# Optimization experiments

Measured on AMD Instinct MI355X. Metric: run time of the kernel, lower is better.

## Reference

```python
import jax, jax.numpy as jnp
import numpy as np

IMG_SIZE = 224
ALPHA = 100.0  # hardcoded softmax temperature in knnsearch_t_grad


def _sqdist(a, b):
    # (B,N,C),(B,M,C) -> (B,N,M) squared euclidean distances
    return (jnp.sum(a * a, -1)[:, :, None]
            - 2.0 * jnp.einsum('bnc,bmc->bnm', a, b)
            + jnp.sum(b * b, -1)[:, None, :])


def _cdist(a, b):
    return jnp.sqrt(jnp.maximum(_sqdist(a, b), 1e-12))


def proj2img(pc, img_offset):
    # faithful jax port of GraphDeformLoss_Neural_Partial.proj2img
    B, N, _ = pc.shape
    pc_max = pc.max(axis=1)              # (B,3)
    pc_min_full = pc.min(axis=1)         # (B,3)
    pc_range = pc_max - pc_min_full
    grid_size = pc_range[:, :2].max(axis=-1) / (IMG_SIZE - 3)   # (B,)
    pc_min = pc_min_full[:, None, :2]                            # (B,1,2)
    gs = grid_size[:, None, None]
    idx_xy = jnp.floor((pc[:, :, :2] - pc_min) / gs)             # (B,N,2)
    # densify each point into a 5x5 neighborhood of pixels
    idx_dense = (idx_xy[:, :, None, :] + img_offset[None, None]).reshape(B, N * 25, 2) + 1.0
    center = jnp.floor((idx_dense.max(axis=1) + idx_dense.min(axis=1)) / 2.0)  # (B,2)
    offset = IMG_SIZE / 2.0 - center - 1.0                       # (B,2) = (offset_x, offset_y)
    idx_off = idx_dense + offset[:, None, :]
    # boundary correction as in the torch code, plus clip for safety
    idx_off = idx_off + (idx_off < 0).astype(jnp.float32) - (idx_off > IMG_SIZE - 1).astype(jnp.float32)
    idx_off = jnp.clip(idx_off, 0, IMG_SIZE - 1)
    f_dense = jnp.repeat(jnp.repeat(pc[:, :, None, 2:3], 25, axis=2).reshape(B, N * 25, 1), 3, axis=-1)
    flat = (idx_off[..., 0] * IMG_SIZE + idx_off[..., 1]).astype(jnp.int32)   # (B,N*25)
    out = jax.vmap(lambda f, i: jax.ops.segment_sum(f, i, num_segments=IMG_SIZE * IMG_SIZE))(f_dense, flat)
    img = out.reshape(B, IMG_SIZE, IMG_SIZE, 3).transpose(0, 3, 1, 2)  # (B,3,H,W)
    return jax.nn.sigmoid(img)


def setup_inputs() -> dict:
    key = jax.random.key(0)
    k1, k2, k3, k4 = jax.random.split(key, 4)
    B, N, M, C = 4, 4995, 4995, 128
    off = jnp.array([[i, j] for i in range(-2, 3) for j in range(-2, 3)], dtype=jnp.float32)
    return {
        'verts1': jax.random.normal(k1, (B, N, 3), jnp.float32),
        'verts2': jax.random.normal(k2, (B, M, 3), jnp.float32),
        'feat1': jax.random.normal(k3, (B, N, C), jnp.float32),
        'feat2': jax.random.normal(k4, (B, M, C), jnp.float32),
        'img_offset': off,
        'k': 10,
    }


def reference(verts1, verts2, feat1, feat2, img_offset, k):
    # knnsearch_t_grad: soft correspondence from feature-space cdist + softmax
    d_feat = _cdist(feat1, feat2)                               # (B,N,M)
    Pi_12 = jax.nn.softmax(-ALPHA * d_feat, axis=-1)
    verts12 = jnp.einsum('bnm,bmc->bnc', Pi_12, verts2)         # pulled-back points (B,N,3)
    # chamfer (squared distances, as chamfer_3DDist); partial: take dist1 branch (N<=M)
    d2 = _sqdist(verts12, verts2)
    self_rec_loss = jnp.mean(jnp.min(d2, axis=-1))
    # knn_grad + index_points: gather k-NN features on source cloud
    d2_11 = _sqdist(verts1, verts1)
    _, idx11 = jax.lax.top_k(-d2_11, k)                         # (B,N,k) nearest
    feat1_conv = jax.vmap(lambda p, i: p[i])(feat1, idx11)      # (B,N,k,C)
    deform_feat_loss = jnp.mean((feat1_conv - feat1[:, :, None, :]) ** 2)
    # point-to-image projection loss
    img1 = proj2img(verts12, img_offset)
    img2 = proj2img(verts2, img_offset)
    img_loss = jnp.mean((img1 - img2) ** 2)
    return self_rec_loss + img_loss + deform_feat_loss
```

## Files before the change

kernel.cpp:

```cpp
#include <hip/hip_runtime.h>
#include <math.h>

#define BB 4
#define NN 4995
#define CC 128
#define IMG 224
#define IMGP (IMG*IMG)
#define ALPHA_F 100.0f
#define SPLITS 8
#define COLS_PER_SPLIT 640
#define RBLK 40
#define NG 158
#define NTAP (2*BB*NN*25)
#define NREP 4
#define TKCAP 256

#define SM_SCALE 20813.6898f
#define NEG2S   -41627.3796f
#define EPS_S    2.08136898e-8f

#define OFF_V12    0
#define OFF_FN1    60000
#define OFF_V1Q    81000
#define OFF_V2Q    161000
#define OFF_C2Q    241000
#define OFF_PART   321000
#define OFF_IMG1   1121000
#define OFF_IMG2   1321704
#define OFF_ACC    1522408
#define OFF_STATS  1522792
#define OFF_PADQ   1522920
#define OFF_F2H    1523000
#define OFF_F2L    2818000
#define OFF_IMGR   4113000
#define WS_NEED_REP ((size_t)5719000*sizeof(float))
#define ZERO_START OFF_IMG1
#define ZERO_FLOATS (1522920 - OFF_IMG1)

typedef short v8s  __attribute__((ext_vector_type(8)));
typedef float v16f __attribute__((ext_vector_type(16)));

#if __has_builtin(__builtin_amdgcn_exp2f)
__device__ __forceinline__ float fast_exp2(float x){ return __builtin_amdgcn_exp2f(x); }
#else
__device__ __forceinline__ float fast_exp2(float x){ float r; asm("v_exp_f32 %0, %1" : "=v"(r) : "v"(x)); return r; }
#endif
#if __has_builtin(__builtin_amdgcn_sqrtf)
__device__ __forceinline__ float fast_sqrt(float x){ return __builtin_amdgcn_sqrtf(x); }
#else
__device__ __forceinline__ float fast_sqrt(float x){ float r; asm("v_sqrt_f32 %0, %1" : "=v"(r) : "v"(x)); return r; }
#endif

__device__ __forceinline__ float wave_min(float v){
#pragma unroll
  for (int off=32; off; off>>=1) v = fminf(v, __shfl_xor(v, off));
  return v;
}
__device__ __forceinline__ float wave_sum(float v){
#pragma unroll
  for (int off=32; off; off>>=1) v += __shfl_xor(v, off);
  return v;
}

__device__ __forceinline__ int pack_bf_hi(float a, float b){
  return (int)__builtin_amdgcn_perm(__float_as_uint(b), __float_as_uint(a), 0x07060302u);
}

__device__ __forceinline__ void cvt_hilo(float4 a, float4 c, int4& hi, int4& lo){
  float hx=__uint_as_float(__float_as_uint(a.x)&0xffff0000u);
  float hy=__uint_as_float(__float_as_uint(a.y)&0xffff0000u);
  float hz=__uint_as_float(__float_as_uint(a.z)&0xffff0000u);
  float hw=__uint_as_float(__float_as_uint(a.w)&0xffff0000u);
  float gx=__uint_as_float(__float_as_uint(c.x)&0xffff0000u);
  float gy=__uint_as_float(__float_as_uint(c.y)&0xffff0000u);
  float gz=__uint_as_float(__float_as_uint(c.z)&0xffff0000u);
  float gw=__uint_as_float(__float_as_uint(c.w)&0xffff0000u);
  hi = make_int4(pack_bf_hi(a.x,a.y), pack_bf_hi(a.z,a.w),
                 pack_bf_hi(c.x,c.y), pack_bf_hi(c.z,c.w));
  lo = make_int4(pack_bf_hi(a.x-hx,a.y-hy), pack_bf_hi(a.z-hz,a.w-hw),
                 pack_bf_hi(c.x-gx,c.y-gy), pack_bf_hi(c.z-gz,c.w-gw));
}

__device__ __forceinline__ v8s i4_to_s8(int4 v){
  union { int4 i; v8s s; } u; u.i = v; return u.s;
}

__device__ __forceinline__ void gld_lds16(const void* g, void* l){
  __builtin_amdgcn_global_load_lds((const __attribute__((address_space(1))) void*)g,
                                   (__attribute__((address_space(3))) void*)l, 16, 0, 0);
}

__device__ __forceinline__ unsigned int fkey(float f){
  unsigned int u = __float_as_uint(f);
  return ((int)u < 0) ? ~u : (u ^ 0x80000000u);
}

__global__ __launch_bounds__(256) void k_norms(const float* __restrict__ verts1, const float* __restrict__ verts2,
                        const float* __restrict__ feat1, const float* __restrict__ feat2,
                        float* __restrict__ ws) {
  int gt = blockIdx.x*blockDim.x + threadIdx.x;
  int i = gt >> 2, sub = gt & 3;
  if (i >= BB*NN) return;
  const float4* fa = (const float4*)(feat1 + (size_t)i*CC) + sub*8;
  const float4* fb = (const float4*)(feat2 + (size_t)i*CC) + sub*8;
  float s1=0.f, s2=0.f;
#pragma unroll
  for (int k=0;k<8;k++){
    float4 t = fa[k];
    s1 = fmaf(t.x,t.x,s1); s1 = fmaf(t.y,t.y,s1); s1 = fmaf(t.z,t.z,s1); s1 = fmaf(t.w,t.w,s1);
    float4 u = fb[k];
    s2 = fmaf(u.x,u.x,s2); s2 = fmaf(u.y,u.y,s2); s2 = fmaf(u.z,u.z,s2); s2 = fmaf(u.w,u.w,s2);
  }
  s1 += __shfl_xor(s1,1); s1 += __shfl_xor(s1,2);
  s2 += __shfl_xor(s2,1); s2 += __shfl_xor(s2,2);
  if (sub == 0){
    float x=verts1[(size_t)i*3], y=verts1[(size_t)i*3+1], z=verts1[(size_t)i*3+2];
    ((float4*)(ws+OFF_V1Q))[i] = make_float4(x,y,z, x*x+y*y+z*z);
    float x2=verts2[(size_t)i*3], y2=verts2[(size_t)i*3+1], z2=verts2[(size_t)i*3+2];
    ((float4*)(ws+OFF_V2Q))[i] = make_float4(x2,y2,z2, x2*x2+y2*y2+z2*z2);
    ((float4*)(ws+OFF_C2Q))[i] = make_float4(x2,y2,z2, SM_SCALE*s2);
    ws[OFF_FN1+i] = SM_SCALE*s1;
  }
  if (gt == 0)
    *((float4*)(ws+OFF_PADQ)) = make_float4(0.f,0.f,0.f,1e30f);
}

__global__ __launch_bounds__(256) void k_conv(const float* __restrict__ feat2, float* __restrict__ ws) {
  int g = blockIdx.x, b = blockIdx.y;
  int t = threadIdx.x;
  int q = t >> 5, c32 = t & 31;
  int col = g*32 + c32; if (col > NN-1) col = NN-1;
  const float4* src = (const float4*)(feat2 + ((size_t)(b*NN + col))*CC) + q*4;
  float4 v0 = src[0], v1 = src[1], v2 = src[2], v3 = src[3];
  short* f2h = (short*)(ws + OFF_F2H);
  short* f2l = (short*)(ws + OFF_F2L);
  size_t base = ((size_t)(b*NG + g))*4096 + (size_t)q*512 + c32*8;
  int4 hi, lo;
  cvt_hilo(v0, v1, hi, lo);
  *(int4*)&f2h[base] = hi;  *(int4*)&f2l[base] = lo;
  cvt_hilo(v2, v3, hi, lo);
  *(int4*)&f2h[base + 256] = hi;  *(int4*)&f2l[base + 256] = lo;
}

__global__ __launch_bounds__(256) void k_stageA(const float* __restrict__ feat1,
      float* __restrict__ ws) {
  __shared__ __align__(16) short Bbuf[2][4096];
  __shared__ __align__(16) float colq[768*4];

  int rblk  = blockIdx.x;
  int split = blockIdx.y;
  int b     = blockIdx.z;
  int rowBase = rblk*128;
  int colBase = split*COLS_PER_SPLIT;
  int colEnd  = colBase + COLS_PER_SPLIT; if (colEnd > NN) colEnd = NN;
  int nct = (colEnd - colBase + 63) >> 6;
  int nst = nct << 2;

  int t    = threadIdx.x;
  int w    = t >> 6;
  int lane = t & 63;
  int half = lane >> 5;
  int m32  = lane & 31;

  const float* f1b = feat1 + (size_t)b*NN*CC;
  const short* f2h = (const short*)(ws + OFF_F2H);
  const short* f2l = (const short*)(ws + OFF_F2L);
  const float4* c2q = (const float4*)(ws + OFF_C2Q) + (size_t)b*NN;
  const float4* padq = (const float4*)(ws + OFF_PADQ);

#pragma unroll
  for (int r=0; r<3; r++){
    int col = colBase + r*256 + t;
    const float4* src = (col < NN) ? (c2q + col) : padq;
    gld_lds16(src, &colq[(r*256 + w*64)*4]);
  }

  size_t f2base = (((size_t)(b*NG) + (colBase>>5) + (w>>1)) << 12) + (size_t)((t&127)*8);

  {
    short* d = &Bbuf[0][0] + w*512;
    gld_lds16(f2h + f2base, d);
    gld_lds16(f2l + f2base, d + 2048);
  }

  int nrow = rowBase + w*32 + m32;
  int nclamp = nrow > NN-1 ? NN-1 : nrow;
  float sn = ws[OFF_FN1 + (size_t)b*NN + nclamp];
  const float4* ar = (const float4*)(f1b + (size_t)nclamp*CC) + (half<<1);
  v8s Afh[8], Afl[8];
#pragma unroll
  for (int sl=0; sl<8; ++sl){
    float4 v0 = ar[sl*4], v1 = ar[sl*4+1];
    int4 hi, lo;
    cvt_hilo(v0, v1, hi, lo);
    Afh[sl] = i4_to_s8(hi); Afl[sl] = i4_to_s8(lo);
  }

  __syncthreads();

  float mm = INFINITY, S = 0.f, Vx = 0.f, Vy = 0.f, Vz = 0.f;

  for (int ci = 0; ci < nct; ci++){
    v16f acc0, acc1;
#pragma unroll
    for (int i=0;i<16;i++){ acc0[i]=0.f; acc1[i]=0.f; }

#pragma unroll
    for (int kt = 0; kt < 4; kt++){
      int s = (ci<<2) + kt;
      if (s+1 < nst){
        int s1 = s+1;
        size_t so = f2base + ((size_t)(s1>>2)<<13) + ((size_t)(s1&3)<<10);
        short* d = &Bbuf[0][0] + ((s1&1)<<12) + w*512;
        gld_lds16(f2h + so, d);
        gld_lds16(f2l + so, d + 2048);
      }
      const short* Bh = &Bbuf[0][0] + ((s&1)<<12);
      const short* Bl = Bh + 2048;
#pragma unroll
      for (int kh=0; kh<2; kh++){
        int fo = (kh<<9) + (half<<8) + (m32<<3);
        v8s a0h = *(const v8s*)&Bh[fo];
        v8s a0l = *(const v8s*)&Bl[fo];
        v8s a1h = *(const v8s*)&Bh[1024+fo];
        v8s a1l = *(const v8s*)&Bl[1024+fo];
        v8s b1h = Afh[kt*2+kh];
        v8s b1l = Afl[kt*2+kh];
        __builtin_amdgcn_s_setprio(1);
        acc0 = __builtin_amdgcn_mfma_f32_32x32x16_bf16(a0h, b1h, acc0, 0,0,0);
        acc0 = __builtin_amdgcn_mfma_f32_32x32x16_bf16(a0h, b1l, acc0, 0,0,0);
        acc0 = __builtin_amdgcn_mfma_f32_32x32x16_bf16(a0l, b1h, acc0, 0,0,0);
        acc1 = __builtin_amdgcn_mfma_f32_32x32x16_bf16(a1h, b1h, acc1, 0,0,0);
        acc1 = __builtin_amdgcn_mfma_f32_32x32x16_bf16(a1h, b1l, acc1, 0,0,0);
        acc1 = __builtin_amdgcn_mfma_f32_32x32x16_bf16(a1l, b1h, acc1, 0,0,0);
        __builtin_amdgcn_s_setprio(0);
      }
      __syncthreads();
    }

    int cb4 = ci<<8;
    float Mt = INFINITY;
#pragma unroll
    for (int reg=0; reg<16; reg++){
      int cp0 = (reg&3) + 8*(reg>>2) + 4*half;
      float f0 = colq[cb4 + cp0*4 + 3];
      float d0 = fmaf(NEG2S, acc0[reg], sn) + f0;
      float p0 = fast_sqrt(fmaxf(d0, EPS_S));
      acc0[reg] = p0; Mt = fminf(Mt, p0);
      float f1v = colq[cb4 + (cp0+32)*4 + 3];
      float d1 = fmaf(NEG2S, acc1[reg], sn) + f1v;
      float p1 = fast_sqrt(fmaxf(d1, EPS_S));
      acc1[reg] = p1; Mt = fminf(Mt, p1);
    }
    float mn = fminf(mm, Mt);
    float sc = fast_exp2(mn - mm);
    float se=0.f, sx=0.f, sy=0.f, sz=0.f;
#pragma unroll
    for (int reg=0; reg<16; reg++){
      int cp0 = (reg&3) + 8*(reg>>2) + 4*half;
      float4 q0 = *(const float4*)&colq[cb4 + cp0*4];
      float e0 = fast_exp2(mn - acc0[reg]);
      se += e0; sx=fmaf(e0,q0.x,sx); sy=fmaf(e0,q0.y,sy); sz=fmaf(e0,q0.z,sz);
      float4 q1 = *(const float4*)&colq[cb4 + (cp0+32)*4];
      float e1 = fast_exp2(mn - acc1[reg]);
      se += e1; sx=fmaf(e1,q1.x,sx); sy=fmaf(e1,q1.y,sy); sz=fmaf(e1,q1.z,sz);
    }
    S  = fmaf(S,  sc, se);
    Vx = fmaf(Vx, sc, sx);
    Vy = fmaf(Vy, sc, sy);
    Vz = fmaf(Vz, sc, sz);
    mm = mn;
  }

  {
    float m2  = __shfl_xor(mm, 32);
    float S2  = __shfl_xor(S,  32);
    float Vx2 = __shfl_xor(Vx, 32);
    float Vy2 = __shfl_xor(Vy, 32);
    float Vz2 = __shfl_xor(Vz, 32);
    float M = fminf(mm, m2);
    float c1 = fast_exp2(M - mm), c2 = fast_exp2(M - m2);
    float Sf  = S*c1  + S2*c2;
    float Vxf = Vx*c1 + Vx2*c2;
    float Vyf = Vy*c1 + Vy2*c2;
    float Vzf = Vz*c1 + Vz2*c2;
    if (half==0 && nrow < NN){
      float* p = ws + OFF_PART + ((size_t)(b*NN+nrow)*SPLITS + split)*5;
      p[0]=M; p[1]=Sf; p[2]=Vxf; p[3]=Vyf; p[4]=Vzf;
    }
  }
}

__global__ void k_combine(float* __restrict__ ws) {
  int row = blockIdx.x*blockDim.x + threadIdx.x;
  if (row >= BB*NN) return;
  const float* p = ws + OFF_PART + (size_t)row*SPLITS*5;
  float mm = INFINITY;
#pragma unroll
  for (int s=0;s<SPLITS;s++) mm = fminf(mm, p[s*5]);
  float S=0.f,Vx=0.f,Vy=0.f,Vz=0.f;
#pragma unroll
  for (int s=0;s<SPLITS;s++){
    float sc = fast_exp2(mm - p[s*5]);
    S  += p[s*5+1]*sc; Vx += p[s*5+2]*sc; Vy += p[s*5+3]*sc; Vz += p[s*5+4]*sc;
  }
  ws[OFF_V12+(size_t)row*3+0]=Vx/S;
  ws[OFF_V12+(size_t)row*3+1]=Vy/S;
  ws[OFF_V12+(size_t)row*3+2]=Vz/S;
}

__global__ __launch_bounds__(256) void k_selfrec(float* __restrict__ ws) {
  int rblk = blockIdx.x, b = blockIdx.y;
  int lane = threadIdx.x & 63, w = threadIdx.x >> 6;
  int r0 = rblk*16 + w*4;
  const float4* v2q = (const float4*)(ws + OFF_V2Q) + (size_t)b*NN;
  const float* v12 = ws + OFF_V12 + (size_t)b*NN*3;
  float xr[4], yr[4], zr[4], sar[4]; bool val[4];
#pragma unroll
  for (int j=0;j<4;j++){
    int n = r0+j; val[j] = (n < NN); int nc = val[j] ? n : NN-1;
    float x=v12[(size_t)nc*3], y=v12[(size_t)nc*3+1], z=v12[(size_t)nc*3+2];
    sar[j]=x*x+y*y+z*z;
    xr[j]=-2.0f*x; yr[j]=-2.0f*y; zr[j]=-2.0f*z;
  }
  float mn0=INFINITY, mn1=INFINITY, mn2=INFINITY, mn3=INFINITY;
  for (int m=lane; m<NN; m+=64) {
    float4 q = v2q[m];
    mn0 = fminf(mn0, fmaf(xr[0],q.x, fmaf(yr[0],q.y, fmaf(zr[0],q.z, q.w))));
    mn1 = fminf(mn1, fmaf(xr[1],q.x, fmaf(yr[1],q.y, fmaf(zr[1],q.z, q.w))));
    mn2 = fminf(mn2, fmaf(xr[2],q.x, fmaf(yr[2],q.y, fmaf(zr[2],q.z, q.w))));
    mn3 = fminf(mn3, fmaf(xr[3],q.x, fmaf(yr[3],q.y, fmaf(zr[3],q.z, q.w))));
  }
  mn0 = wave_min(mn0); mn1 = wave_min(mn1); mn2 = wave_min(mn2); mn3 = wave_min(mn3);
  float s = (val[0]?(mn0+sar[0]):0.f) + (val[1]?(mn1+sar[1]):0.f)
          + (val[2]?(mn2+sar[2]):0.f) + (val[3]?(mn3+sar[3]):0.f);
  if (lane==0)
    atomicAdd(((double*)(ws+OFF_ACC)) + ((rblk*4 + w) & 63), (double)s);
}

__global__ __launch_bounds__(256, 4) void k_topk(const float* __restrict__ feat1,
        const int* __restrict__ kptr, float* __restrict__ ws) {
  __shared__ unsigned int keybuf[4*256];
  __shared__ unsigned long long cand[4*TKCAP];
  __shared__ int scnt[4];
  __shared__ float tfs[4];
  __shared__ int sel[4][16];
  __shared__ float rs[4];
  int t = threadIdx.x;
  int lane = t & 63, wid = t >> 6;
  int b = blockIdx.y;
  int n0 = blockIdx.x*4;
  int kk = *kptr; if (kk > 16) kk = 16; if (kk < 1) kk = 1;

  const float4* v1q = (const float4*)(ws + OFF_V1Q) + (size_t)b*NN;
  float mx[4], my2[4], mz[4], sa_unused;
  (void)sa_unused;
#pragma unroll
  for (int j=0;j<4;j++){
    int n = n0+j; if (n > NN-1) n = NN-1;
    float4 me = v1q[n];
    mx[j]=-2.0f*me.x; my2[j]=-2.0f*me.y; mz[j]=-2.0f*me.z;
  }
  if (t < 4) scnt[t] = 0;

  float e2[20][4];
  float mn[4] = {INFINITY, INFINITY, INFINITY, INFINITY};
#pragma unroll
  for (int i=0;i<19;i++){
    int m = t + 256*i;
    float4 q = v1q[m];
#pragma unroll
    for (int j=0;j<4;j++){
      float d = fmaf(mx[j], q.x, fmaf(my2[j], q.y, fmaf(mz[j], q.z, q.w)));
      e2[i][j] = d; mn[j] = fminf(mn[j], d);
    }
  }
  {
    int m = t + 256*19;
    bool ok = (m < NN);
    float4 q = v1q[ok ? m : NN-1];
#pragma unroll
    for (int j=0;j<4;j++){
      float d = fmaf(mx[j], q.x, fmaf(my2[j], q.y, fmaf(mz[j], q.z, q.w)));
      d = ok ? d : 1e30f;
      e2[19][j] = d; mn[j] = fminf(mn[j], d);
    }
  }

#pragma unroll
  for (int j=0;j<4;j++)
    keybuf[j*256 + t] = fkey(mn[j]) >> 16;
  __syncthreads();

  {
    unsigned int k0 = keybuf[wid*256 + lane];
    unsigned int k1 = keybuf[wid*256 + 64 + lane];
    unsigned int k2 = keybuf[wid*256 + 128 + lane];
    unsigned int k3 = keybuf[wid*256 + 192 + lane];
    unsigned int prefix = 0;
    for (int bit=15; bit>=0; --bit){
      unsigned int piv = prefix | (1u<<bit);
      int c = __popcll(__ballot(k0 < piv)) + __popcll(__ballot(k1 < piv))
            + __popcll(__ballot(k2 < piv)) + __popcll(__ballot(k3 < piv));
      if (c < kk) prefix = piv;
    }
    unsigned int K = (prefix<<16) | 0xFFFFu;
    unsigned int fb = (K & 0x80000000u) ? (K ^ 0x80000000u) : ~K;
    if (lane==0) tfs[wid] = __uint_as_float(fb);
  }
  __syncthreads();
  float tff[4] = {tfs[0], tfs[1], tfs[2], tfs[3]};

#pragma unroll
  for (int i=0;i<20;i++){
    int m = t + 256*i;
#pragma unroll
    for (int j=0;j<4;j++){
      if (e2[i][j] <= tff[j]){
        int pos = atomicAdd(&scnt[j], 1);
        if (pos < TKCAP)
          cand[j*TKCAP + pos] = ((unsigned long long)fkey(e2[i][j]) << 13) | (unsigned int)m;
      }
    }
  }
  __syncthreads();

  {
    int cnt = scnt[wid]; if (cnt > TKCAP) cnt = TKCAP;
    unsigned long long kv0 = (lane       < cnt) ? cand[wid*TKCAP + lane]       : ~0ull;
    unsigned long long kv1 = (lane + 64  < cnt) ? cand[wid*TKCAP + lane + 64]  : ~0ull;
    unsigned long long kv2 = (lane + 128 < cnt) ? cand[wid*TKCAP + lane + 128] : ~0ull;
    unsigned long long kv3 = (lane + 192 < cnt) ? cand[wid*TKCAP + lane + 192] : ~0ull;
    int r0=0, r1=0, r2=0, r3=0;
    for (int q2=0; q2<cnt; ++q2){
      unsigned long long cj = cand[wid*TKCAP + q2];
      r0 += (cj < kv0); r1 += (cj < kv1); r2 += (cj < kv2); r3 += (cj < kv3);
    }
    if (lane       < cnt && r0 < kk) sel[wid][r0] = (int)(kv0 & 8191ull);
    if (lane + 64  < cnt && r1 < kk) sel[wid][r1] = (int)(kv1 & 8191ull);
    if (lane + 128 < cnt && r2 < kk) sel[wid][r2] = (int)(kv2 & 8191ull);
    if (lane + 192 < cnt && r3 < kk) sel[wid][r3] = (int)(kv3 & 8191ull);
  }
  __syncthreads();

  float mse = 0.f;
  int c = t & 127;
  int rh = t >> 7;
  for (int j=0;j<4;j++){
    int n = n0+j;
    if (n >= NN) break;
    const float* f1n = feat1 + ((size_t)b*NN + n)*CC;
    float e = f1n[c];
    for (int r=rh; r<kk; r+=2){
      const float* g = feat1 + ((size_t)b*NN + sel[j][r])*CC;
      float d = g[c]-e;
      mse = fmaf(d,d,mse);
    }
  }

  float acc = wave_sum(mse);
  if (lane==0) rs[wid] = acc;
  __syncthreads();
  if (t==0){
    float s = (rs[0]+rs[1])+(rs[2]+rs[3]);
    atomicAdd(((double*)(ws+OFF_ACC)) + 128 + ((blockIdx.x + b) & 63), (double)s);
  }
}

__global__ void k_imgstats(const float* __restrict__ verts2, const float* __restrict__ imgoff,
                           float* __restrict__ ws) {
  __shared__ float r0[4], r1[4], r2[4], r3[4];
  __shared__ float sgs, smnx, smny;
  int img = blockIdx.x >> 2, b = blockIdx.x & 3;
  const float* pc = (img==0) ? (ws + OFF_V12 + (size_t)b*NN*3) : (verts2 + (size_t)b*NN*3);
  int lane = threadIdx.x & 63, wid = threadIdx.x >> 6;
  float mnx=INFINITY, mxx=-INFINITY, mny=INFINITY, mxy=-INFINITY;
  for (int n = threadIdx.x; n < NN; n += 256) {
    float x = pc[(size_t)n*3], y = pc[(size_t)n*3+1];
    mnx=fminf(mnx,x); mxx=fmaxf(mxx,x); mny=fminf(mny,y); mxy=fmaxf(mxy,y);
  }
#pragma unroll
  for (int off=32; off; off>>=1) {
    mnx=fminf(mnx,__shfl_xor(mnx,off)); mxx=fmaxf(mxx,__shfl_xor(mxx,off));
    mny=fminf(mny,__shfl_xor(mny,off)); mxy=fmaxf(mxy,__shfl_xor(mxy,off));
  }
  if (lane==0){ r0[wid]=mnx; r1[wid]=mxx; r2[wid]=mny; r3[wid]=mxy; }
  __syncthreads();
  float* st = ws + OFF_STATS + (size_t)(img*4+b)*16;
  if (threadIdx.x==0){
    mnx=fminf(fminf(r0[0],r0[1]),fminf(r0[2],r0[3]));
    mxx=fmaxf(fmaxf(r1[0],r1[1]),fmaxf(r1[2],r1[3]));
    mny=fminf(fminf(r2[0],r2[1]),fminf(r2[2],r2[3]));
    mxy=fmaxf(fmaxf(r3[0],r3[1]),fmaxf(r3[2],r3[3]));
    float gs = fmaxf(mxx-mnx, mxy-mny) / 221.0f;
    sgs=gs; smnx=mnx; smny=mny;
    st[0]=mnx; st[1]=mxx; st[2]=mny; st[3]=mxy; st[4]=gs;
  }
  __syncthreads();
  float gs=sgs, bx=smnx, by=smny;
  float fmnx=INFINITY, fmxx=-INFINITY, fmny=INFINITY, fmxy=-INFINITY;
  for (int n = threadIdx.x; n < NN; n += 256) {
    float fx = floorf((pc[(size_t)n*3]-bx)/gs);
    float fy = floorf((pc[(size_t)n*3+1]-by)/gs);
    fmnx=fminf(fmnx,fx); fmxx=fmaxf(fmxx,fx); fmny=fminf(fmny,fy); fmxy=fmaxf(fmxy,fy);
  }
#pragma unroll
  for (int off=32; off; off>>=1) {
    fmnx=fminf(fmnx,__shfl_xor(fmnx,off)); fmxx=fmaxf(fmxx,__shfl_xor(fmxx,off));
    fmny=fminf(fmny,__shfl_xor(fmny,off)); fmxy=fmaxf(fmxy,__shfl_xor(fmxy,off));
  }
  __syncthreads();
  if (lane==0){ r0[wid]=fmnx; r1[wid]=fmxx; r2[wid]=fmny; r3[wid]=fmxy; }
  __syncthreads();
  if (threadIdx.x==0){
    fmnx=fminf(fminf(r0[0],r0[1]),fminf(r0[2],r0[3]));
    fmxx=fmaxf(fmaxf(r1[0],r1[1]),fmaxf(r1[2],r1[3]));
    fmny=fminf(fminf(r2[0],r2[1]),fminf(r2[2],r2[3]));
    fmxy=fmaxf(fmaxf(r3[0],r3[1]),fmaxf(r3[2],r3[3]));
    float omnx=INFINITY, omxx=-INFINITY, omny=INFINITY, omxy=-INFINITY;
    for (int l=0;l<25;l++){
      float ox=imgoff[l*2], oy=imgoff[l*2+1];
      omnx=fminf(omnx,ox); omxx=fmaxf(omxx,ox); omny=fminf(omny,oy); omxy=fmaxf(omxy,oy);
    }
    float cx = floorf(((fmxx+omxx+1.0f)+(fmnx+omnx+1.0f))*0.5f);
    float cy = floorf(((fmxy+omxy+1.0f)+(fmny+omny+1.0f))*0.5f);
    st[5] = (112.0f - cx) - 1.0f;
    st[6] = (112.0f - cy) - 1.0f;
  }
}

__global__ __launch_bounds__(256) void k_scatter(const float* __restrict__ verts2,
                          const float* __restrict__ imgoff,
                          float* __restrict__ ws, int nrep) {
  int g = blockIdx.x*256 + threadIdx.x;
  if (g >= NTAP) return;
  int p = g / 25; int l = g - p*25;
  int img = p / (BB*NN); int r = p - img*(BB*NN); int b = r / NN;
  const float* pc = (img==0) ? (ws + OFF_V12) : verts2;
  float x = pc[(size_t)r*3], y = pc[(size_t)r*3+1], z = pc[(size_t)r*3+2];
  const float* st = ws + OFF_STATS + (size_t)(img*4+b)*16;
  float mnx=st[0], mny=st[2], gs=st[4], offx=st[5], offy=st[6];
  float bx = floorf((x-mnx)/gs) + 1.0f + offx;
  float by = floorf((y-mny)/gs) + 1.0f + offy;
  float vx = bx + imgoff[l*2], vy = by + imgoff[l*2+1];
  vx += (vx<0.f?1.f:0.f) - (vx>223.f?1.f:0.f);
  vy += (vy<0.f?1.f:0.f) - (vy>223.f?1.f:0.f);
  vx = fminf(fmaxf(vx,0.f),223.f); vy = fminf(fmaxf(vy,0.f),223.f);
  int flat = (int)(vx*224.f + vy);
  float* im;
  if (nrep > 1)
    im = ws + OFF_IMGR + ((size_t)(((blockIdx.x & (nrep-1))*2 + img)*BB + b))*IMGP;
  else
    im = ws + (img==0?OFF_IMG1:OFF_IMG2) + (size_t)b*IMGP;
  atomicAdd(im + flat, z);
}

__global__ void k_imgloss(float* __restrict__ ws, int nrep) {
  int i = blockIdx.x*blockDim.x + threadIdx.x;
  float v = 0.f;
  if (i < BB*IMGP) {
    float a, c;
    if (nrep > 1){
      a = 0.f; c = 0.f;
      for (int r=0; r<nrep; ++r){
        a += ws[OFF_IMGR + (size_t)(r*2+0)*BB*IMGP + i];
        c += ws[OFF_IMGR + (size_t)(r*2+1)*BB*IMGP + i];
      }
    } else {
      a = ws[OFF_IMG1+i]; c = ws[OFF_IMG2+i];
    }
    float sa = 1.f/(1.f+expf(-a)), sc = 1.f/(1.f+expf(-c));
    float d = sa - sc; v = d*d;
  }
  v = wave_sum(v);
  if ((threadIdx.x&63)==0)
    atomicAdd(((double*)(ws+OFF_ACC)) + 64 + (blockIdx.x & 63), (double)v);
}

__global__ void k_final(const int* __restrict__ kptr, const float* __restrict__ ws, float* __restrict__ out) {
  const double* acc = (const double*)(ws+OFF_ACC);
  int t = threadIdx.x;
  double a0 = acc[t], a1 = acc[64+t], a2 = acc[128+t];
#pragma unroll
  for (int off=32; off; off>>=1){
    a0 += __shfl_down(a0, off);
    a1 += __shfl_down(a1, off);
    a2 += __shfl_down(a2, off);
  }
  if (t==0){
    int kk = *kptr; if (kk > 16) kk = 16; if (kk < 1) kk = 1;
    double srl = a0 / (double)(BB*NN);
    double img = a1 / ((double)BB*IMGP);
    double df  = a2 / ((double)BB*NN*kk*CC);
    out[0] = (float)(srl + img + df);
  }
}

extern "C" void kernel_launch(void* const* d_in, const int* in_sizes, int n_in,
                              void* d_out, int out_size, void* d_ws, size_t ws_size,
                              hipStream_t stream) {
  (void)in_sizes; (void)n_in; (void)out_size;
  const float* verts1 = (const float*)d_in[0];
  const float* verts2 = (const float*)d_in[1];
  const float* feat1  = (const float*)d_in[2];
  const float* feat2  = (const float*)d_in[3];
  const float* imgoff = (const float*)d_in[4];
  const int*   kptr   = (const int*)d_in[5];
  float* ws  = (float*)d_ws;
  float* out = (float*)d_out;
  int nrep = (ws_size >= WS_NEED_REP) ? NREP : 1;

  hipMemsetAsync(ws + ZERO_START, 0, (size_t)ZERO_FLOATS*sizeof(float), stream);
  if (nrep > 1)
    hipMemsetAsync(ws + OFF_IMGR, 0, (size_t)NREP*2*BB*IMGP*sizeof(float), stream);

  k_norms<<<(BB*NN*4+255)/256, 256, 0, stream>>>(verts1, verts2, feat1, feat2, ws);

  dim3 gC(NG, BB);
  k_conv<<<gC, 256, 0, stream>>>(feat2, ws);

  dim3 gA(RBLK, SPLITS, BB);
  k_stageA<<<gA, 256, 0, stream>>>(feat1, ws);
  k_combine<<<(BB*NN+255)/256, 256, 0, stream>>>(ws);

  dim3 gS((NN+15)/16, BB);
  k_selfrec<<<gS, 256, 0, stream>>>(ws);

  dim3 gT((NN+3)/4, BB);
  k_topk<<<gT, 256, 0, stream>>>(feat1, kptr, ws);

  k_imgstats<<<8, 256, 0, stream>>>(verts2, imgoff, ws);
  k_scatter<<<(NTAP+255)/256, 256, 0, stream>>>(verts2, imgoff, ws, nrep);
  k_imgloss<<<(BB*IMGP+255)/256, 256, 0, stream>>>(ws, nrep);

  k_final<<<1,64,0,stream>>>(kptr, ws, out);
}
```

Baseline: 353.3 us.

## Deepen stageA B-tile prefetch to four LDS buffers, widen selfrec rows per wave

k_stageA moves from a double-buffered LDS ring with one prefetch and a __syncthreads per k-step to a four-slot ring that keeps three tiles in flight. Synchronisation is now a manual vmcnt wait plus s_barrier, and the A-fragment loads are issued before the B prefetch. This aims to hide global-to-LDS latency behind the MFMA work, at the cost of more LDS per block and reliance on the hand-set vmcnt count being correct. Separately, k_selfrec now processes 8 rows per wave instead of 4, halving the grid and reusing each loaded verts2 point across more rows.

```diff
diff --git a/kernel.cpp b/kernel.cpp
--- a/kernel.cpp
+++ b/kernel.cpp
@@ -144,7 +144,7 @@
 
 __global__ __launch_bounds__(256) void k_stageA(const float* __restrict__ feat1,
       float* __restrict__ ws) {
-  __shared__ __align__(16) short Bbuf[2][4096];
+  __shared__ __align__(16) short Bbuf[4][4096];
   __shared__ __align__(16) float colq[768*4];
 
   int rblk  = blockIdx.x;
@@ -168,21 +168,6 @@
   const float4* c2q = (const float4*)(ws + OFF_C2Q) + (size_t)b*NN;
   const float4* padq = (const float4*)(ws + OFF_PADQ);
 
-#pragma unroll
-  for (int r=0; r<3; r++){
-    int col = colBase + r*256 + t;
-    const float4* src = (col < NN) ? (c2q + col) : padq;
-    gld_lds16(src, &colq[(r*256 + w*64)*4]);
-  }
-
-  size_t f2base = (((size_t)(b*NG) + (colBase>>5) + (w>>1)) << 12) + (size_t)((t&127)*8);
-
-  {
-    short* d = &Bbuf[0][0] + w*512;
-    gld_lds16(f2h + f2base, d);
-    gld_lds16(f2l + f2base, d + 2048);
-  }
-
   int nrow = rowBase + w*32 + m32;
   int nclamp = nrow > NN-1 ? NN-1 : nrow;
   float sn = ws[OFF_FN1 + (size_t)b*NN + nclamp];
@@ -195,8 +180,27 @@
     cvt_hilo(v0, v1, hi, lo);
     Afh[sl] = i4_to_s8(hi); Afl[sl] = i4_to_s8(lo);
   }
-
-  __syncthreads();
+  asm volatile("" :: "v"(sn));
+#pragma unroll
+  for (int sl=0; sl<8; ++sl)
+    asm volatile("" :: "v"(Afh[sl]), "v"(Afl[sl]));
+
+#pragma unroll
+  for (int r=0; r<3; r++){
+    int col = colBase + r*256 + t;
+    const float4* src = (col < NN) ? (c2q + col) : padq;
+    gld_lds16(src, &colq[(r*256 + w*64)*4]);
+  }
+
+  size_t f2base = (((size_t)(b*NG) + (colBase>>5) + (w>>1)) << 12) + (size_t)((t&127)*8);
+
+#pragma unroll
+  for (int T=0; T<3; ++T){
+    size_t so = f2base + ((size_t)(T>>2)<<13) + ((size_t)(T&3)<<10);
+    short* d = &Bbuf[T][0] + w*512;
+    gld_lds16(f2h + so, d);
+    gld_lds16(f2l + so, d + 2048);
+  }
 
   float mm = INFINITY, S = 0.f, Vx = 0.f, Vy = 0.f, Vz = 0.f;
 
@@ -207,15 +211,19 @@
 
 #pragma unroll
     for (int kt = 0; kt < 4; kt++){
-      int s = (ci<<2) + kt;
-      if (s+1 < nst){
-        int s1 = s+1;
-        size_t so = f2base + ((size_t)(s1>>2)<<13) + ((size_t)(s1&3)<<10);
-        short* d = &Bbuf[0][0] + ((s1&1)<<12) + w*512;
+      __builtin_amdgcn_sched_barrier(0);
+      asm volatile("s_waitcnt vmcnt(4)" ::: "memory");
+      __builtin_amdgcn_s_barrier();
+
+      int T = (ci<<2) + kt + 3;
+      if (T < nst){
+        size_t so = f2base + ((size_t)(T>>2)<<13) + ((size_t)(T&3)<<10);
+        short* d = &Bbuf[(kt+3)&3][0] + w*512;
         gld_lds16(f2h + so, d);
         gld_lds16(f2l + so, d + 2048);
       }
-      const short* Bh = &Bbuf[0][0] + ((s&1)<<12);
+
+      const short* Bh = &Bbuf[kt][0];
       const short* Bl = Bh + 2048;
 #pragma unroll
       for (int kh=0; kh<2; kh++){
@@ -235,7 +243,6 @@
         acc1 = __builtin_amdgcn_mfma_f32_32x32x16_bf16(a1l, b1h, acc1, 0,0,0);
         __builtin_amdgcn_s_setprio(0);
       }
-      __syncthreads();
     }
 
     int cb4 = ci<<8;
@@ -312,28 +319,32 @@
 __global__ __launch_bounds__(256) void k_selfrec(float* __restrict__ ws) {
   int rblk = blockIdx.x, b = blockIdx.y;
   int lane = threadIdx.x & 63, w = threadIdx.x >> 6;
-  int r0 = rblk*16 + w*4;
+  int r0 = rblk*32 + w*8;
   const float4* v2q = (const float4*)(ws + OFF_V2Q) + (size_t)b*NN;
   const float* v12 = ws + OFF_V12 + (size_t)b*NN*3;
-  float xr[4], yr[4], zr[4], sar[4]; bool val[4];
-#pragma unroll
-  for (int j=0;j<4;j++){
+  float xr[8], yr[8], zr[8], sar[8]; bool val[8];
+#pragma unroll
+  for (int j=0;j<8;j++){
     int n = r0+j; val[j] = (n < NN); int nc = val[j] ? n : NN-1;
     float x=v12[(size_t)nc*3], y=v12[(size_t)nc*3+1], z=v12[(size_t)nc*3+2];
     sar[j]=x*x+y*y+z*z;
     xr[j]=-2.0f*x; yr[j]=-2.0f*y; zr[j]=-2.0f*z;
   }
-  float mn0=INFINITY, mn1=INFINITY, mn2=INFINITY, mn3=INFINITY;
+  float mn[8];
+#pragma unroll
+  for (int j=0;j<8;j++) mn[j] = INFINITY;
   for (int m=lane; m<NN; m+=64) {
     float4 q = v2q[m];
-    mn0 = fminf(mn0, fmaf(xr[0],q.x, fmaf(yr[0],q.y, fmaf(zr[0],q.z, q.w))));
-    mn1 = fminf(mn1, fmaf(xr[1],q.x, fmaf(yr[1],q.y, fmaf(zr[1],q.z, q.w))));
-    mn2 = fminf(mn2, fmaf(xr[2],q.x, fmaf(yr[2],q.y, fmaf(zr[2],q.z, q.w))));
-    mn3 = fminf(mn3, fmaf(xr[3],q.x, fmaf(yr[3],q.y, fmaf(zr[3],q.z, q.w))));
-  }
-  mn0 = wave_min(mn0); mn1 = wave_min(mn1); mn2 = wave_min(mn2); mn3 = wave_min(mn3);
-  float s = (val[0]?(mn0+sar[0]):0.f) + (val[1]?(mn1+sar[1]):0.f)
-          + (val[2]?(mn2+sar[2]):0.f) + (val[3]?(mn3+sar[3]):0.f);
+#pragma unroll
+    for (int j=0;j<8;j++)
+      mn[j] = fminf(mn[j], fmaf(xr[j],q.x, fmaf(yr[j],q.y, fmaf(zr[j],q.z, q.w))));
+  }
+  float s = 0.f;
+#pragma unroll
+  for (int j=0;j<8;j++){
+    float v = wave_min(mn[j]);
+    s += val[j] ? (v + sar[j]) : 0.f;
+  }
   if (lane==0)
     atomicAdd(((double*)(ws+OFF_ACC)) + ((rblk*4 + w) & 63), (double)s);
 }
@@ -353,8 +364,7 @@
   int kk = *kptr; if (kk > 16) kk = 16; if (kk < 1) kk = 1;
 
   const float4* v1q = (const float4*)(ws + OFF_V1Q) + (size_t)b*NN;
-  float mx[4], my2[4], mz[4], sa_unused;
-  (void)sa_unused;
+  float mx[4], my2[4], mz[4];
 #pragma unroll
   for (int j=0;j<4;j++){
     int n = n0+j; if (n > NN-1) n = NN-1;
@@ -623,7 +633,7 @@
   k_stageA<<<gA, 256, 0, stream>>>(feat1, ws);
   k_combine<<<(BB*NN+255)/256, 256, 0, stream>>>(ws);
 
-  dim3 gS((NN+15)/16, BB);
+  dim3 gS((NN+31)/32, BB);
   k_selfrec<<<gS, 256, 0, stream>>>(ws);
 
   dim3 gT((NN+3)/4, BB);
```

Result: no change. 359.0 us (+1.6%).
